# Kernel tuning notes

Hardware: AMD Instinct MI355X
Metric: run time of the kernel (lower is better)

Reference implementation:

```python
import jax, jax.numpy as jnp
import numpy as np

HEADS = 12
DIM_HEAD = 64
INNER = HEADS * DIM_HEAD  # 768
DIM = 512
KS = 3


def setup_inputs() -> dict:
    key = jax.random.key(0)
    ks = jax.random.split(key, 5)
    B, H, W = 8, 32, 32
    N = H * W + 1  # +1 cls token -> has_cls path
    x = jax.random.normal(ks[0], (B, N, DIM), dtype=jnp.float32)
    w_qkv = jax.random.normal(ks[1], (3 * INNER, DIM), dtype=jnp.float32) * (DIM ** -0.5)
    w_dw = jax.random.normal(ks[2], (DIM, 1, KS, KS), dtype=jnp.float32) * (1.0 / KS)
    w_out = jax.random.normal(ks[3], (DIM, INNER), dtype=jnp.float32) * (INNER ** -0.5)
    b_out = jax.random.normal(ks[4], (DIM,), dtype=jnp.float32) * 0.01
    return {"x": x, "w_qkv": w_qkv, "w_dw": w_dw, "w_out": w_out,
            "b_out": b_out, "h_feat": H, "w_feat": W}


def reference(x, w_qkv, w_dw, w_out, b_out, h_feat, w_feat):
    B, N, C = x.shape
    scale = DIM_HEAD ** -0.5
    # qkv projection (Linear, no bias): torch weight layout (out,in)
    qkv = jnp.einsum('bnc,oc->bno', x, w_qkv)  # (B,N,3*INNER)
    q, k, v = jnp.split(qkv, 3, axis=-1)

    def split_heads(t):
        return t.reshape(B, N, HEADS, DIM_HEAD).transpose(0, 2, 1, 3)  # (B,H,N,d)

    q, k, v = map(split_heads, (q, k, v))
    dots = jnp.einsum('bhid,bhjd->bhij', q, k) * scale
    attn = jax.nn.softmax(dots, axis=-1)
    out_attn = jnp.einsum('bhij,bhjd->bhid', attn, v)
    out_attn = out_attn.transpose(0, 2, 1, 3).reshape(B, N, INNER)

    has_cls = (N == h_feat * w_feat + 1)  # static
    spatial = x[:, 1:, :] if has_cls else x
    spatial_2d = spatial.transpose(0, 2, 1).reshape(B, C, h_feat, w_feat)
    # depthwise conv, padding = ks//2 (SAME for odd ks, stride 1)
    loc = jax.lax.conv_general_dilated(
        spatial_2d, w_dw, window_strides=(1, 1), padding='SAME',
        feature_group_count=C,
        dimension_numbers=('NCHW', 'OIHW', 'NCHW'))
    local_out = loc.reshape(B, C, h_feat * w_feat).transpose(0, 2, 1)  # (B,hw,C)
    if has_cls:
        cls_out = x[:, :1, :INNER]  # C < INNER so this is the full cls token
        local_out = jnp.concatenate([cls_out, local_out], axis=1)  # (B,N,C)
    if local_out.shape[-1] < INNER:
        out = out_attn + jnp.pad(
            local_out, ((0, 0), (0, 0), (0, INNER - local_out.shape[-1])))
    else:
        out = out_attn
    # output Linear (dropout=0 in eval)
    return jnp.einsum('bni,oi->bno', out, w_out) + b_out
```

## Files before the change

### kernel.cpp

```cpp
#include <hip/hip_runtime.h>
#include <hip/hip_bf16.h>
#include <stdint.h>
#include <math.h>

typedef __bf16 bf16;
typedef __bf16 bf16x8 __attribute__((ext_vector_type(8)));
typedef float f32x4 __attribute__((ext_vector_type(4)));
typedef short s4 __attribute__((ext_vector_type(4)));

#define QSCALE 0.1803368801111f


__device__ __forceinline__ void gload_lds16(const void* g, void* l) {
  typedef const __attribute__((address_space(1))) char g_char;
  typedef __attribute__((address_space(3))) char l_char;
  g_char* gp = (g_char*)(uintptr_t)g;
  l_char* lp = (l_char*)(uint32_t)(uintptr_t)l;
  __builtin_amdgcn_global_load_lds(gp, lp, 16, 0, 0);
}

__device__ __forceinline__ float fexp2(float x) {
#if __has_builtin(__builtin_amdgcn_exp2f)
  return __builtin_amdgcn_exp2f(x);
#else
  return exp2f(x);
#endif
}

__device__ __forceinline__ float frcp(float x) {
#if __has_builtin(__builtin_amdgcn_rcpf)
  return __builtin_amdgcn_rcpf(x);
#else
  return 1.f / x;
#endif
}

__device__ __forceinline__ uint32_t pk2(float a, float b) {
  union { bf16 h; unsigned short u; } ua, ub;
  ua.h = (bf16)a; ub.h = (bf16)b;
  return (uint32_t)ua.u | ((uint32_t)ub.u << 16);
}

__device__ __forceinline__ f32x4 pv_mfma(s4 a, s4 b, f32x4 c) {
#if __has_builtin(__builtin_amdgcn_mfma_f32_16x16x16bf16_1k)
  return __builtin_amdgcn_mfma_f32_16x16x16bf16_1k(a, b, c, 0, 0, 0);
#else
  asm volatile("v_mfma_f32_16x16x16_bf16 %0, %1, %2, %0" : "+v"(c) : "v"(a), "v"(b));
  return c;
#endif
}

__global__ __launch_bounds__(256) void k_prep(const float* __restrict__ x,
                                              const float* __restrict__ wqkv,
                                              const float* __restrict__ wout,
                                              bf16* __restrict__ xb, bf16* __restrict__ wqkvb,
                                              bf16* __restrict__ woutb, bf16* __restrict__ vP) {
  int i = blockIdx.x * 256 + threadIdx.x;
  const float* src = nullptr;
  bf16* dst = nullptr;
  int q = i;
  bool zero = false;
  if (i < 1064960) {
    if (i < 1049600) src = x; else zero = true;
    dst = xb;
  } else if (i < 1064960 + 294912) {
    q = i - 1064960; src = wqkv; dst = wqkvb;
  } else if (i < 1064960 + 294912 + 98304) {
    q = i - (1064960 + 294912); src = wout; dst = woutb;
  } else {
    int qq = i - (1064960 + 294912 + 98304);
    int z = qq * 4;
    int head = z >> 12;
    int off = z & 4095;
    uint2 zz; zz.x = 0u; zz.y = 0u;
    *(uint2*)&vP[(size_t)head * 69632 + 65536 + off] = zz;
    return;
  }
  float4 v = make_float4(0.f, 0.f, 0.f, 0.f);
  if (!zero) v = *(const float4*)&src[(size_t)q * 4];
  uint2 p;
  p.x = pk2(v.x, v.y);
  p.y = pk2(v.z, v.w);
  *(uint2*)&dst[(size_t)q * 4] = p;
}

template <int EPI, int BN>
__global__ __launch_bounds__(256) void k_gemm(const bf16* __restrict__ A,
                                              const bf16* __restrict__ Bt, int K,
                                              bf16* __restrict__ q, bf16* __restrict__ kk,
                                              bf16* __restrict__ vt,
                                              const float* __restrict__ bias,
                                              float* __restrict__ out) {
  __shared__ __attribute__((aligned(16))) bf16 sA[128 * 64];
  __shared__ __attribute__((aligned(16))) bf16 sB[BN * 64];
  constexpr int MF = (BN == 128) ? 4 : 2;
  constexpr int WROWS = (BN == 128) ? 64 : 32;
  const int tid = threadIdx.x;
  const int lane = tid & 63;
  const int w = tid >> 6;
  const int wr = (BN == 128) ? (w >> 1) : w;
  const int wc = (BN == 128) ? (w & 1) : 0;
  const int tn = blockIdx.x, tm = blockIdx.y;
  const int l15 = lane & 15, l4 = lane >> 4;
  const int srow = lane >> 3, sslot = lane & 7;

  f32x4 acc[MF][4] = {};

  const int Ksteps = K >> 6;
  for (int kt = 0; kt < Ksteps; ++kt) {
    __syncthreads();
#pragma unroll
    for (int i = 0; i < 4; ++i) {
      int row = w * 32 + i * 8 + srow;
      int clog = sslot ^ (row & 7);
      gload_lds16(A + ((size_t)(tm * 128 + row) * K + kt * 64 + clog * 8),
                  &sA[(w * 32 + i * 8) * 64]);
    }
#pragma unroll
    for (int i = 0; i < BN / 32; ++i) {
      int row = w * (BN / 4) + i * 8 + srow;
      int clog = sslot ^ (row & 7);
      gload_lds16(Bt + ((size_t)(tn * BN + row) * K + kt * 64 + clog * 8),
                  &sB[(w * (BN / 4) + i * 8) * 64]);
    }
    __syncthreads();
#pragma unroll
    for (int ks = 0; ks < 2; ++ks) {
      bf16x8 af[MF], bfr[4];
#pragma unroll
      for (int mf = 0; mf < MF; ++mf) {
        int row = wr * WROWS + mf * 16 + l15;
        int phys = (ks * 4 + l4) ^ (row & 7);
        af[mf] = *(const bf16x8*)&sA[row * 64 + phys * 8];
      }
#pragma unroll
      for (int nf = 0; nf < 4; ++nf) {
        int row = wc * 64 + nf * 16 + l15;
        int phys = (ks * 4 + l4) ^ (row & 7);
        bfr[nf] = *(const bf16x8*)&sB[row * 64 + phys * 8];
      }
#pragma unroll
      for (int mf = 0; mf < MF; ++mf)
#pragma unroll
        for (int nf = 0; nf < 4; ++nf)
          acc[mf][nf] =
              __builtin_amdgcn_mfma_f32_16x16x32_bf16(af[mf], bfr[nf], acc[mf][nf], 0, 0, 0);
    }
  }

  const int Rbase = tm * 128 + wr * WROWS + l4 * 4;
  const int Cbase = tn * BN + wc * 64 + l15;
#pragma unroll
  for (int mf = 0; mf < MF; ++mf) {
    int R0 = Rbase + mf * 16;
    if (R0 >= 8200) continue;
    if (EPI == 0) {
      int b = R0 / 1025;
      int n0 = R0 - b * 1025;
      bool sb = (n0 + 3 <= 1024);
      bool sbv = sb && ((n0 & 3) == 0);
#pragma unroll
      for (int nf = 0; nf < 4; ++nf) {
        int Cc = Cbase + nf * 16;
        int seg = (Cc >= 1536) ? 2 : (Cc >= 768 ? 1 : 0);
        int inner = Cc - seg * 768;
        int h = inner >> 6, d = inner & 63;
        if (seg == 2) {
          if (sbv) {
            uint2 p;
            p.x = pk2(acc[mf][nf][0], acc[mf][nf][1]);
            p.y = pk2(acc[mf][nf][2], acc[mf][nf][3]);
            *(uint2*)&vt[(((size_t)(b * 12 + h) * 272 + (n0 >> 2)) * 64 + d) * 4] = p;
          } else {
#pragma unroll
            for (int r = 0; r < 4; ++r) {
              int R = R0 + r;
              int b2 = R / 1025;
              int n = R - b2 * 1025;
              vt[(((size_t)(b2 * 12 + h) * 272 + (n >> 2)) * 64 + d) * 4 + (n & 3)] =
                  (bf16)acc[mf][nf][r];
            }
          }
        } else {
          bf16* dst = seg ? kk : q;
          float scl = seg ? 1.f : QSCALE;
#pragma unroll
          for (int r = 0; r < 4; ++r) {
            int b2, n;
            if (sb) { b2 = b; n = n0 + r; }
            else { int R = R0 + r; b2 = R / 1025; n = R - b2 * 1025; }
            dst[(((size_t)b2 * 12 + h) * 1088 + n) * 64 + d] = (bf16)(acc[mf][nf][r] * scl);
          }
        }
      }
    } else {
#pragma unroll
      for (int r = 0; r < 4; ++r) {
        int R = R0 + r;
#pragma unroll
        for (int nf = 0; nf < 4; ++nf) {
          int Cc = Cbase + nf * 16;
          out[(size_t)R * 512 + Cc] = acc[mf][nf][r] + bias[Cc];
        }
      }
    }
  }
}

__global__ __launch_bounds__(256) void k_flash(const bf16* __restrict__ qg,
                                               const bf16* __restrict__ kg,
                                               const bf16* __restrict__ vpg,
                                               bf16* __restrict__ outb) {
  __shared__ __attribute__((aligned(16))) bf16 sK[2][64 * 64];
  __shared__ __attribute__((aligned(16))) bf16 sVP[2][16 * 256];
  const int tid = threadIdx.x, lane = tid & 63, w = tid >> 6;
  const int l15 = lane & 15, l4 = lane >> 4;
  const int wg = blockIdx.x;
  const int logical = (wg & 7) * 108 + (wg >> 3);
  const int bh = logical / 9, qgp = logical - bh * 9;
  const int b = bh / 12, h = bh - b * 12;
  const int srow = lane >> 3, sslot = lane & 7;
  const int nsub = (qgp == 8) ? 1 : 2;

  bf16x8 qf[2][2];
#pragma unroll
  for (int s = 0; s < 2; ++s) {
    if (s < nsub) {
      size_t qoff = ((size_t)bh * 1088 + (qgp * 2 + s) * 64 + w * 16 + l15) * 64 + l4 * 8;
      qf[s][0] = *(const bf16x8*)&qg[qoff];
      qf[s][1] = *(const bf16x8*)&qg[qoff + 32];
    }
  }

  float mreg[2] = {-INFINITY, -INFINITY};
  float lreg[2] = {0.f, 0.f};
  f32x4 oa[2][4] = {};

  const int px0 = (l4 ^ (l15 & 7)) * 8;
  const int px1 = ((4 + l4) ^ (l15 & 7)) * 8;

  auto STAGE = [&](int bi, int t) {
    int row = w * 16 + srow;
    int clog = sslot ^ (row & 7);
    gload_lds16(kg + ((size_t)bh * 1088 + t * 64 + row) * 64 + clog * 8, &sK[bi][row * 64]);
    int row2 = row + 8;
    int clog2 = sslot ^ (row2 & 7);
    gload_lds16(kg + ((size_t)bh * 1088 + t * 64 + row2) * 64 + clog2 * 8, &sK[bi][row2 * 64]);
    size_t eb = (size_t)bh * 69632 + (size_t)t * 4096;
    int lo = w * 1024 + lane * 8;
    gload_lds16(vpg + eb + lo, &sVP[bi][lo]);
    gload_lds16(vpg + eb + 512 + lo, &sVP[bi][512 + lo]);
  };

  STAGE(0, 0);
  int cur = 0;

  for (int t = 0; t < 17; ++t) {
    asm volatile("s_waitcnt vmcnt(0)" ::: "memory");
    __builtin_amdgcn_s_barrier();
    __builtin_amdgcn_sched_barrier(0);
    if (t < 16) STAGE(cur ^ 1, t + 1);

    const bf16* kb_ = sK[cur];
    const bf16* vpb = sVP[cur];

    bf16x8 af[2][4];
    s4 vfr[4][4];
#pragma unroll
    for (int jt = 0; jt < 4; ++jt) {
      af[0][jt] = *(const bf16x8*)&kb_[(jt * 16 + l15) * 64 + px0];
      af[1][jt] = *(const bf16x8*)&kb_[(jt * 16 + l15) * 64 + px1];
#pragma unroll
      for (int db = 0; db < 4; ++db)
        vfr[jt][db] = *(const s4*)&vpb[((jt * 4 + l4) * 64 + db * 16 + l15) * 4];
    }

#pragma unroll
    for (int s = 0; s < 2; ++s) {
      if (s >= nsub) continue;
      f32x4 sc[4] = {};
      __builtin_amdgcn_s_setprio(1);
#pragma unroll
      for (int ks = 0; ks < 2; ++ks)
#pragma unroll
        for (int jt = 0; jt < 4; ++jt)
          sc[jt] = __builtin_amdgcn_mfma_f32_16x16x32_bf16(af[ks][jt], qf[s][ks], sc[jt], 0, 0, 0);
      __builtin_amdgcn_s_setprio(0);

      if (t == 16) {
#pragma unroll
        for (int jt = 0; jt < 4; ++jt)
#pragma unroll
          for (int r = 0; r < 4; ++r) {
            if (jt == 0 && r == 0)
              sc[jt][r] = (l4 == 0) ? sc[jt][r] : -INFINITY;
            else
              sc[jt][r] = -INFINITY;
          }
      }

      float pm = fmaxf(fmaxf(fmaxf(sc[0][0], sc[0][1]), fmaxf(sc[0][2], sc[0][3])),
                       fmaxf(fmaxf(sc[1][0], sc[1][1]), fmaxf(sc[1][2], sc[1][3])));
      float pm2 = fmaxf(fmaxf(fmaxf(sc[2][0], sc[2][1]), fmaxf(sc[2][2], sc[2][3])),
                        fmaxf(fmaxf(sc[3][0], sc[3][1]), fmaxf(sc[3][2], sc[3][3])));
      pm = fmaxf(pm, pm2);
      pm = fmaxf(pm, __shfl_xor(pm, 16));
      pm = fmaxf(pm, __shfl_xor(pm, 32));

      if (__any(pm > mreg[s] + 8.0f)) {
        float mn = fmaxf(mreg[s], pm);
        float alpha = fexp2(mreg[s] - mn);
        mreg[s] = mn;
        lreg[s] *= alpha;
        float ar[4];
#pragma unroll
        for (int r = 0; r < 4; ++r) ar[r] = __shfl(alpha, l4 * 4 + r);
#pragma unroll
        for (int db = 0; db < 4; ++db)
#pragma unroll
          for (int r = 0; r < 4; ++r) oa[s][db][r] *= ar[r];
      }
      float mn = mreg[s];

      union { uint32_t u[2]; s4 v; } pa[4];
      float lsum = 0.f;
#pragma unroll
      for (int jt = 0; jt < 4; ++jt) {
        float p0 = fexp2(sc[jt][0] - mn);
        float p1 = fexp2(sc[jt][1] - mn);
        float p2 = fexp2(sc[jt][2] - mn);
        float p3 = fexp2(sc[jt][3] - mn);
        lsum += (p0 + p1) + (p2 + p3);
        pa[jt].u[0] = pk2(p0, p1);
        pa[jt].u[1] = pk2(p2, p3);
      }
      lreg[s] += lsum;

      __builtin_amdgcn_s_setprio(1);
#pragma unroll
      for (int jt = 0; jt < 4; ++jt)
#pragma unroll
        for (int db = 0; db < 4; ++db)
          oa[s][db] = pv_mfma(pa[jt].v, vfr[jt][db], oa[s][db]);
      __builtin_amdgcn_s_setprio(0);
    }
    cur ^= 1;
  }

#pragma unroll
  for (int s = 0; s < 2; ++s) {
    if (s >= nsub) continue;
    float ls = lreg[s];
    ls += __shfl_xor(ls, 16);
    ls += __shfl_xor(ls, 32);
    float linv = frcp(ls);
#pragma unroll
    for (int r = 0; r < 4; ++r) {
      float ir = __shfl(linv, l4 * 4 + r);
      int n = (qgp * 2 + s) * 64 + w * 16 + l4 * 4 + r;
      if (n >= 1025) continue;
#pragma unroll
      for (int db = 0; db < 4; ++db)
        outb[((size_t)b * 1025 + n) * 768 + h * 64 + db * 16 + l15] = (bf16)(oa[s][db][r] * ir);
    }
  }
}

__global__ __launch_bounds__(256) void k_local(const float* __restrict__ x,
                                               const float* __restrict__ wdw,
                                               bf16* __restrict__ outb) {
  const int b = blockIdx.x, y = blockIdx.y, xseg = blockIdx.z, c0 = threadIdx.x;
  const int x0 = xseg * 8;
  const bool hm = (y > 0), hp = (y < 31);
#pragma unroll
  for (int hf = 0; hf < 2; ++hf) {
    const int c = hf * 256 + c0;
    float w9[9];
#pragma unroll
    for (int k = 0; k < 9; ++k) w9[k] = wdw[(size_t)c * 9 + k];
    const float* xb = x + ((size_t)b * 1025 + 1) * 512 + c;
    float A = 0.f, Bp = 0.f;
    for (int cc = x0 - 1; cc <= x0 + 8; ++cc) {
      float v0 = 0.f, v1 = 0.f, v2 = 0.f;
      if (cc >= 0 && cc < 32) {
        v1 = xb[((size_t)y * 32 + cc) * 512];
        if (hm) v0 = xb[((size_t)(y - 1) * 32 + cc) * 512];
        if (hp) v2 = xb[((size_t)(y + 1) * 32 + cc) * 512];
      }
      float t0 = v0 * w9[0] + v1 * w9[3] + v2 * w9[6];
      float t1 = v0 * w9[1] + v1 * w9[4] + v2 * w9[7];
      float t2 = v0 * w9[2] + v1 * w9[5] + v2 * w9[8];
      int oc = cc - 1;
      if (oc >= x0 && oc <= x0 + 7) {
        float acc = A + t2;
        size_t o = ((size_t)b * 1025 + 1 + y * 32 + oc) * 768 + c;
        outb[o] = (bf16)((float)outb[o] + acc);
      }
      A = Bp + t1;
      Bp = t0;
    }
  }
  if (y == 0 && xseg == 0) {
#pragma unroll
    for (int hf = 0; hf < 2; ++hf) {
      int c = hf * 256 + c0;
      size_t o = ((size_t)b * 1025) * 768 + c;
      outb[o] = (bf16)((float)outb[o] + x[((size_t)b * 1025) * 512 + c]);
    }
  }
}

extern "C" void kernel_launch(void* const* d_in, const int* in_sizes, int n_in,
                              void* d_out, int out_size, void* d_ws, size_t ws_size,
                              hipStream_t stream) {
  const float* x = (const float*)d_in[0];
  const float* w_qkv = (const float*)d_in[1];
  const float* w_dw = (const float*)d_in[2];
  const float* w_out = (const float*)d_in[3];
  const float* b_out = (const float*)d_in[4];
  float* out = (float*)d_out;

  char* ws = (char*)d_ws;
  size_t off = 0;
  auto alloc = [&](size_t bytes) {
    char* p = ws + off;
    off = (off + bytes + 255) & ~(size_t)255;
    return p;
  };
  bf16* xb    = (bf16*)alloc((size_t)8320 * 512 * 2);
  bf16* wqkvb = (bf16*)alloc((size_t)2304 * 512 * 2);
  bf16* woutb = (bf16*)alloc((size_t)512 * 768 * 2);
  bf16* qb    = (bf16*)alloc((size_t)96 * 1088 * 64 * 2);
  bf16* kb    = (bf16*)alloc((size_t)96 * 1088 * 64 * 2);
  bf16* vP    = (bf16*)alloc((size_t)96 * 272 * 64 * 4 * 2);
  bf16* outb  = (bf16*)alloc((size_t)8320 * 768 * 2);

  k_prep<<<6080, 256, 0, stream>>>(x, w_qkv, w_out, xb, wqkvb, woutb, vP);
  k_gemm<0, 128><<<dim3(18, 65), 256, 0, stream>>>(xb, wqkvb, 512, qb, kb, vP, nullptr, nullptr);
  k_flash<<<864, 256, 0, stream>>>(qb, kb, vP, outb);
  k_local<<<dim3(8, 32, 4), 256, 0, stream>>>(x, w_dw, outb);
  k_gemm<1, 64><<<dim3(8, 65), 256, 0, stream>>>(outb, woutb, 768, nullptr, nullptr, nullptr,
                                                 b_out, out);
}
```

Baseline: 158.2 us.

## Split flash attention workgroups to one 64-row query tile each

Each flash-attention workgroup now handles a single 64-row query tile instead of two, so the grid grows from 864 to 1632 workgroups and per-thread register state halves. K/V tiles are now loaded from LDS just before use instead of being hoisted into registers, and the staging address math is precomputed outside the loop. This aims for more occupancy and better load balance, and it drops the uneven last group that had only one tile. The cost is that each K/V tile is streamed from global memory into LDS twice as often, with less reuse per load.

After: 148.1 us. -6.4%, faster.

```diff
diff --git a/kernel.cpp b/kernel.cpp
--- a/kernel.cpp
+++ b/kernel.cpp
@@ -216,40 +216,37 @@
   const int tid = threadIdx.x, lane = tid & 63, w = tid >> 6;
   const int l15 = lane & 15, l4 = lane >> 4;
   const int wg = blockIdx.x;
-  const int logical = (wg & 7) * 108 + (wg >> 3);
-  const int bh = logical / 9, qgp = logical - bh * 9;
+  const int logical = (wg & 7) * 204 + (wg >> 3);
+  const int bh = logical / 17, qgp = logical - bh * 17;
   const int b = bh / 12, h = bh - b * 12;
   const int srow = lane >> 3, sslot = lane & 7;
-  const int nsub = (qgp == 8) ? 1 : 2;
-
-  bf16x8 qf[2][2];
-#pragma unroll
-  for (int s = 0; s < 2; ++s) {
-    if (s < nsub) {
-      size_t qoff = ((size_t)bh * 1088 + (qgp * 2 + s) * 64 + w * 16 + l15) * 64 + l4 * 8;
-      qf[s][0] = *(const bf16x8*)&qg[qoff];
-      qf[s][1] = *(const bf16x8*)&qg[qoff + 32];
-    }
-  }
-
-  float mreg[2] = {-INFINITY, -INFINITY};
-  float lreg[2] = {0.f, 0.f};
-  f32x4 oa[2][4] = {};
+
+  size_t qoff = ((size_t)bh * 1088 + qgp * 64 + w * 16 + l15) * 64 + l4 * 8;
+  const bf16x8 qf0 = *(const bf16x8*)&qg[qoff];
+  const bf16x8 qf1 = *(const bf16x8*)&qg[qoff + 32];
+
+  float mreg = -INFINITY;
+  float lreg = 0.f;
+  f32x4 oa[4] = {};
 
   const int px0 = (l4 ^ (l15 & 7)) * 8;
   const int px1 = ((4 + l4) ^ (l15 & 7)) * 8;
 
+  const int rowA = w * 16 + srow, rowB = rowA + 8;
+  const int clogA = sslot ^ (rowA & 7), clogB = sslot ^ (rowB & 7);
+  const bf16* kS1 = kg + ((size_t)bh * 1088 + rowA) * 64 + clogA * 8;
+  const bf16* kS2 = kg + ((size_t)bh * 1088 + rowB) * 64 + clogB * 8;
+  const bf16* vS1 = vpg + (size_t)bh * 69632 + w * 1024 + lane * 8;
+  const bf16* vS2 = vS1 + 512;
+  const int kD1 = rowA * 64, kD2 = rowB * 64;
+  const int vD1 = w * 1024 + lane * 8, vD2 = vD1 + 512;
+
   auto STAGE = [&](int bi, int t) {
-    int row = w * 16 + srow;
-    int clog = sslot ^ (row & 7);
-    gload_lds16(kg + ((size_t)bh * 1088 + t * 64 + row) * 64 + clog * 8, &sK[bi][row * 64]);
-    int row2 = row + 8;
-    int clog2 = sslot ^ (row2 & 7);
-    gload_lds16(kg + ((size_t)bh * 1088 + t * 64 + row2) * 64 + clog2 * 8, &sK[bi][row2 * 64]);
-    size_t eb = (size_t)bh * 69632 + (size_t)t * 4096;
-    int lo = w * 1024 + lane * 8;
-    gload_lds16(vpg + eb + lo, &sVP[bi][lo]);
-    gload_lds16(vpg + eb + 512 + lo, &sVP[bi][512 + lo]);
+    size_t o = (size_t)t * 4096;
+    gload_lds16(kS1 + o, &sK[bi][kD1]);
+    gload_lds16(kS2 + o, &sK[bi][kD2]);
+    gload_lds16(vS1 + o, &sVP[bi][vD1]);
+    gload_lds16(vS2 + o, &sVP[bi][vD2]);
   };
 
   STAGE(0, 0);
@@ -264,105 +261,93 @@
     const bf16* kb_ = sK[cur];
     const bf16* vpb = sVP[cur];
 
-    bf16x8 af[2][4];
-    s4 vfr[4][4];
+    f32x4 sc[4] = {};
+    __builtin_amdgcn_s_setprio(1);
 #pragma unroll
     for (int jt = 0; jt < 4; ++jt) {
-      af[0][jt] = *(const bf16x8*)&kb_[(jt * 16 + l15) * 64 + px0];
-      af[1][jt] = *(const bf16x8*)&kb_[(jt * 16 + l15) * 64 + px1];
+      bf16x8 a0 = *(const bf16x8*)&kb_[(jt * 16 + l15) * 64 + px0];
+      sc[jt] = __builtin_amdgcn_mfma_f32_16x16x32_bf16(a0, qf0, sc[jt], 0, 0, 0);
+    }
+#pragma unroll
+    for (int jt = 0; jt < 4; ++jt) {
+      bf16x8 a1 = *(const bf16x8*)&kb_[(jt * 16 + l15) * 64 + px1];
+      sc[jt] = __builtin_amdgcn_mfma_f32_16x16x32_bf16(a1, qf1, sc[jt], 0, 0, 0);
+    }
+    __builtin_amdgcn_s_setprio(0);
+
+    if (t == 16) {
+#pragma unroll
+      for (int jt = 0; jt < 4; ++jt)
+#pragma unroll
+        for (int r = 0; r < 4; ++r) {
+          if (jt == 0 && r == 0)
+            sc[jt][r] = (l4 == 0) ? sc[jt][r] : -INFINITY;
+          else
+            sc[jt][r] = -INFINITY;
+        }
+    }
+
+    float pm = fmaxf(fmaxf(fmaxf(sc[0][0], sc[0][1]), fmaxf(sc[0][2], sc[0][3])),
+                     fmaxf(fmaxf(sc[1][0], sc[1][1]), fmaxf(sc[1][2], sc[1][3])));
+    float pm2 = fmaxf(fmaxf(fmaxf(sc[2][0], sc[2][1]), fmaxf(sc[2][2], sc[2][3])),
+                      fmaxf(fmaxf(sc[3][0], sc[3][1]), fmaxf(sc[3][2], sc[3][3])));
+    pm = fmaxf(pm, pm2);
+    pm = fmaxf(pm, __shfl_xor(pm, 16));
+    pm = fmaxf(pm, __shfl_xor(pm, 32));
+
+    if (__any(pm > mreg + 8.0f)) {
+      float mn = fmaxf(mreg, pm);
+      float alpha = fexp2(mreg - mn);
+      mreg = mn;
+      lreg *= alpha;
+      float ar[4];
+#pragma unroll
+      for (int r = 0; r < 4; ++r) ar[r] = __shfl(alpha, l4 * 4 + r);
 #pragma unroll
       for (int db = 0; db < 4; ++db)
-        vfr[jt][db] = *(const s4*)&vpb[((jt * 4 + l4) * 64 + db * 16 + l15) * 4];
-    }
-
-#pragma unroll
-    for (int s = 0; s < 2; ++s) {
-      if (s >= nsub) continue;
-      f32x4 sc[4] = {};
-      __builtin_amdgcn_s_setprio(1);
-#pragma unroll
-      for (int ks = 0; ks < 2; ++ks)
-#pragma unroll
-        for (int jt = 0; jt < 4; ++jt)
-          sc[jt] = __builtin_amdgcn_mfma_f32_16x16x32_bf16(af[ks][jt], qf[s][ks], sc[jt], 0, 0, 0);
-      __builtin_amdgcn_s_setprio(0);
-
-      if (t == 16) {
-#pragma unroll
-        for (int jt = 0; jt < 4; ++jt)
-#pragma unroll
-          for (int r = 0; r < 4; ++r) {
-            if (jt == 0 && r == 0)
-              sc[jt][r] = (l4 == 0) ? sc[jt][r] : -INFINITY;
-            else
-              sc[jt][r] = -INFINITY;
-          }
-      }
-
-      float pm = fmaxf(fmaxf(fmaxf(sc[0][0], sc[0][1]), fmaxf(sc[0][2], sc[0][3])),
-                       fmaxf(fmaxf(sc[1][0], sc[1][1]), fmaxf(sc[1][2], sc[1][3])));
-      float pm2 = fmaxf(fmaxf(fmaxf(sc[2][0], sc[2][1]), fmaxf(sc[2][2], sc[2][3])),
-                        fmaxf(fmaxf(sc[3][0], sc[3][1]), fmaxf(sc[3][2], sc[3][3])));
-      pm = fmaxf(pm, pm2);
-      pm = fmaxf(pm, __shfl_xor(pm, 16));
-      pm = fmaxf(pm, __shfl_xor(pm, 32));
-
-      if (__any(pm > mreg[s] + 8.0f)) {
-        float mn = fmaxf(mreg[s], pm);
-        float alpha = fexp2(mreg[s] - mn);
-        mreg[s] = mn;
-        lreg[s] *= alpha;
-        float ar[4];
-#pragma unroll
-        for (int r = 0; r < 4; ++r) ar[r] = __shfl(alpha, l4 * 4 + r);
-#pragma unroll
-        for (int db = 0; db < 4; ++db)
-#pragma unroll
-          for (int r = 0; r < 4; ++r) oa[s][db][r] *= ar[r];
-      }
-      float mn = mreg[s];
-
-      union { uint32_t u[2]; s4 v; } pa[4];
-      float lsum = 0.f;
-#pragma unroll
-      for (int jt = 0; jt < 4; ++jt) {
-        float p0 = fexp2(sc[jt][0] - mn);
-        float p1 = fexp2(sc[jt][1] - mn);
-        float p2 = fexp2(sc[jt][2] - mn);
-        float p3 = fexp2(sc[jt][3] - mn);
-        lsum += (p0 + p1) + (p2 + p3);
-        pa[jt].u[0] = pk2(p0, p1);
-        pa[jt].u[1] = pk2(p2, p3);
-      }
-      lreg[s] += lsum;
-
-      __builtin_amdgcn_s_setprio(1);
-#pragma unroll
-      for (int jt = 0; jt < 4; ++jt)
-#pragma unroll
-        for (int db = 0; db < 4; ++db)
-          oa[s][db] = pv_mfma(pa[jt].v, vfr[jt][db], oa[s][db]);
-      __builtin_amdgcn_s_setprio(0);
-    }
+#pragma unroll
+        for (int r = 0; r < 4; ++r) oa[db][r] *= ar[r];
+    }
+    float mn = mreg;
+
+    union { uint32_t u[2]; s4 v; } pa[4];
+    float lsum = 0.f;
+#pragma unroll
+    for (int jt = 0; jt < 4; ++jt) {
+      float p0 = fexp2(sc[jt][0] - mn);
+      float p1 = fexp2(sc[jt][1] - mn);
+      float p2 = fexp2(sc[jt][2] - mn);
+      float p3 = fexp2(sc[jt][3] - mn);
+      lsum += (p0 + p1) + (p2 + p3);
+      pa[jt].u[0] = pk2(p0, p1);
+      pa[jt].u[1] = pk2(p2, p3);
+    }
+    lreg += lsum;
+
+    __builtin_amdgcn_s_setprio(1);
+#pragma unroll
+    for (int jt = 0; jt < 4; ++jt)
+#pragma unroll
+      for (int db = 0; db < 4; ++db) {
+        s4 vf = *(const s4*)&vpb[((jt * 4 + l4) * 64 + db * 16 + l15) * 4];
+        oa[db] = pv_mfma(pa[jt].v, vf, oa[db]);
+      }
+    __builtin_amdgcn_s_setprio(0);
     cur ^= 1;
   }
 
-#pragma unroll
-  for (int s = 0; s < 2; ++s) {
-    if (s >= nsub) continue;
-    float ls = lreg[s];
-    ls += __shfl_xor(ls, 16);
-    ls += __shfl_xor(ls, 32);
-    float linv = frcp(ls);
-#pragma unroll
-    for (int r = 0; r < 4; ++r) {
-      float ir = __shfl(linv, l4 * 4 + r);
-      int n = (qgp * 2 + s) * 64 + w * 16 + l4 * 4 + r;
-      if (n >= 1025) continue;
-#pragma unroll
-      for (int db = 0; db < 4; ++db)
-        outb[((size_t)b * 1025 + n) * 768 + h * 64 + db * 16 + l15] = (bf16)(oa[s][db][r] * ir);
-    }
+  float ls = lreg;
+  ls += __shfl_xor(ls, 16);
+  ls += __shfl_xor(ls, 32);
+  float linv = frcp(ls);
+#pragma unroll
+  for (int r = 0; r < 4; ++r) {
+    float ir = __shfl(linv, l4 * 4 + r);
+    int n = qgp * 64 + w * 16 + l4 * 4 + r;
+    if (n >= 1025) continue;
+#pragma unroll
+    for (int db = 0; db < 4; ++db)
+      outb[((size_t)b * 1025 + n) * 768 + h * 64 + db * 16 + l15] = (bf16)(oa[db][r] * ir);
   }
 }
 
@@ -437,7 +422,7 @@
 
   k_prep<<<6080, 256, 0, stream>>>(x, w_qkv, w_out, xb, wqkvb, woutb, vP);
   k_gemm<0, 128><<<dim3(18, 65), 256, 0, stream>>>(xb, wqkvb, 512, qb, kb, vP, nullptr, nullptr);
-  k_flash<<<864, 256, 0, stream>>>(qb, kb, vP, outb);
+  k_flash<<<1632, 256, 0, stream>>>(qb, kb, vP, outb);
   k_local<<<dim3(8, 32, 4), 256, 0, stream>>>(x, w_dw, outb);
   k_gemm<1, 64><<<dim3(8, 65), 256, 0, stream>>>(outb, woutb, 768, nullptr, nullptr, nullptr,
                                                  b_out, out);
```
